# Kernel optimization log

Hardware: AMD Instinct MI355X
Metric: run time of the kernel (lower is better)

The kernel has to match this reference:

```python
import jax, jax.numpy as jnp
import numpy as np

N = 80000       # nodes
E = 1280000     # edges (avg degree 16)
G = 2000        # graphs
NSHAPE, NCOLOR, POSMAX = 16, 16, 1024
HID, OUT, IN_DIM = 64, 2, 40
EPS = 1e-5


def setup_inputs() -> dict:
    key = jax.random.key(0)
    ks = jax.random.split(key, 20)
    f32 = jnp.float32
    return {
        "shape_id": jax.random.randint(ks[0], (N,), 0, NSHAPE),
        "color_id": jax.random.randint(ks[1], (N,), 0, NCOLOR),
        "pos_id": jax.random.randint(ks[2], (N,), 0, POSMAX),
        "edge_index": jax.random.randint(ks[3], (2, E), 0, N),
        "batch": jnp.sort(jax.random.randint(ks[4], (N,), 0, G)),
        "num_graphs": G,
        "shape_tab": jax.random.normal(ks[5], (NSHAPE, 16), f32),
        "color_tab": jax.random.normal(ks[6], (NCOLOR, 16), f32),
        "pos_tab": jax.random.normal(ks[7], (POSMAX, 8), f32),
        "W1l": jax.random.normal(ks[8], (IN_DIM, HID), f32) / np.sqrt(IN_DIM),
        "b1": jnp.zeros((HID,), f32),
        "W1r": jax.random.normal(ks[9], (IN_DIM, HID), f32) / np.sqrt(IN_DIM),
        "g1": jnp.ones((HID,), f32),
        "be1": jnp.zeros((HID,), f32),
        "W2l": jax.random.normal(ks[10], (HID, HID), f32) / np.sqrt(HID),
        "b2": jnp.zeros((HID,), f32),
        "W2r": jax.random.normal(ks[11], (HID, HID), f32) / np.sqrt(HID),
        "g2": jnp.ones((HID,), f32),
        "be2": jnp.zeros((HID,), f32),
        "Wout": jax.random.normal(ks[12], (HID, OUT), f32) / np.sqrt(HID),
        "bout": jnp.zeros((OUT,), f32),
    }


def sage_conv(x, src, dst, Wl, b, Wr, n_nodes):
    # PyG SAGEConv (mean aggr): out = lin_l(mean_{j in N(i)} x_j) + lin_r(x_i)
    agg = jax.ops.segment_sum(x[src], dst, num_segments=n_nodes)     # [N, F]
    deg = jax.ops.segment_sum(jnp.ones((src.shape[0], 1), x.dtype), dst,
                              num_segments=n_nodes)                  # [N, 1]
    agg = agg / jnp.maximum(deg, 1.0)
    return agg @ Wl + b + x @ Wr


def batch_norm(x, gamma, beta):
    # training-mode BatchNorm1d over nodes
    m = x.mean(axis=0)
    v = x.var(axis=0)
    return (x - m) * (gamma / jnp.sqrt(v + EPS)) + beta


def reference(shape_id, color_id, pos_id, edge_index, batch, num_graphs,
              shape_tab, color_tab, pos_tab,
              W1l, b1, W1r, g1, be1,
              W2l, b2, W2r, g2, be2,
              Wout, bout):
    n_nodes = shape_id.shape[0]
    src, dst = edge_index[0], edge_index[1]
    x = jnp.concatenate([shape_tab[shape_id], color_tab[color_id],
                         pos_tab[pos_id]], axis=-1)                  # [N, 40]
    x = jax.nn.relu(batch_norm(sage_conv(x, src, dst, W1l, b1, W1r, n_nodes), g1, be1))
    # dropout: eval mode -> identity
    x = jax.nn.relu(batch_norm(sage_conv(x, src, dst, W2l, b2, W2r, n_nodes), g2, be2))
    # global mean pool over batch segments
    summed = jax.ops.segment_sum(x, batch, num_segments=num_graphs)   # [G, H]
    counts = jax.ops.segment_sum(jnp.ones((n_nodes, 1), x.dtype), batch,
                                 num_segments=num_graphs)
    pooled = summed / jnp.maximum(counts, 1.0)
    return pooled @ Wout + bout                                       # [G, 2]
```

## Files before the change

kernel.cpp:

```cpp
#include <hip/hip_runtime.h>

#define NN 80000
#define NE 1280000
#define NG 2000
#define HID 64
#define FIN1 40
#define NBUK ((NN + 127) >> 7)
#define BIN_PER 4096
constexpr float EPS = 1e-5f;

typedef _Float16 f16;
typedef f16 f16x4 __attribute__((ext_vector_type(4)));
typedef f16 f16x8 __attribute__((ext_vector_type(8)));
typedef float f32x4 __attribute__((ext_vector_type(4)));

__global__ void embed16(const int* __restrict__ sid, const int* __restrict__ cid,
                        const int* __restrict__ pid,
                        const float* __restrict__ stab, const float* __restrict__ ctab,
                        const float* __restrict__ ptab, f16* __restrict__ x0) {
    int idx = blockIdx.x * 256 + threadIdx.x;
    if (idx >= NN * 5) return;
    int n = idx / 5, u = idx - n * 5;
    const float* srcp;
    if (u < 2)      srcp = &stab[sid[n] * 16 + u * 8];
    else if (u < 4) srcp = &ctab[cid[n] * 16 + (u - 2) * 8];
    else            srcp = &ptab[pid[n] * 8];
    f16x8 o;
#pragma unroll
    for (int i = 0; i < 8; i++) o[i] = (f16)srcp[i];
    *(f16x8*)&x0[(size_t)n * FIN1 + u * 8] = o;
}

__global__ void wprep(const float* __restrict__ W1l, const float* __restrict__ W1r,
                      const float* __restrict__ W2l, const float* __restrict__ W2r,
                      f16* __restrict__ Bt1, f16* __restrict__ Bt2) {
    int i = blockIdx.x * 256 + threadIdx.x;
    if (i < 64 * 104) {
        int j = i / 104, k = i - j * 104;
        float v = 0.f;
        if (k < 40) v = W1l[k * 64 + j];
        else if (k < 80) v = W1r[(k - 40) * 64 + j];
        Bt1[i] = (f16)v;
    }
    int i2 = i - 64 * 104;
    if (i2 >= 0 && i2 < 64 * 136) {
        int j = i2 / 136, k = i2 - j * 136;
        float v = 0.f;
        if (k < 64) v = W2l[k * 64 + j];
        else if (k < 128) v = W2r[(k - 64) * 64 + j];
        Bt2[i2] = (f16)v;
    }
}

__global__ void bucket_hist(const int* __restrict__ dst, int* __restrict__ bcnt) {
    __shared__ int lh[NBUK];
    for (int i = threadIdx.x; i < NBUK; i += 256) lh[i] = 0;
    __syncthreads();
    int e0 = blockIdx.x * BIN_PER;
    int e1 = min(e0 + BIN_PER, NE);
    for (int e = e0 + threadIdx.x; e < e1; e += 256) atomicAdd(&lh[dst[e] >> 7], 1);
    __syncthreads();
    for (int i = threadIdx.x; i < NBUK; i += 256)
        if (lh[i]) atomicAdd(&bcnt[i], lh[i]);
}

__global__ void bucket_scan(const int* __restrict__ bcnt, int* __restrict__ bstart,
                            int* __restrict__ bcur) {
    __shared__ int l[1024];
    int t = threadIdx.x;
    l[t] = (t < NBUK) ? bcnt[t] : 0;
    __syncthreads();
    for (int off = 1; off < 1024; off <<= 1) {
        int v = (t >= off) ? l[t - off] : 0;
        __syncthreads();
        l[t] += v;
        __syncthreads();
    }
    int excl = (t == 0) ? 0 : l[t - 1];
    if (t < NBUK) { bstart[t] = excl; bcur[t] = excl; }
    if (t == NBUK) bstart[NBUK] = NE;
}

__global__ void bin_edges(const int* __restrict__ src, const int* __restrict__ dst,
                          int* __restrict__ bcur, int* __restrict__ ebuf) {
    __shared__ int lh[NBUK];
    __shared__ int lbase[NBUK];
    for (int i = threadIdx.x; i < NBUK; i += 256) lh[i] = 0;
    __syncthreads();
    int e0 = blockIdx.x * BIN_PER;
    int e1 = min(e0 + BIN_PER, NE);
    for (int e = e0 + threadIdx.x; e < e1; e += 256) atomicAdd(&lh[dst[e] >> 7], 1);
    __syncthreads();
    for (int i = threadIdx.x; i < NBUK; i += 256) {
        int c = lh[i];
        lbase[i] = c ? atomicAdd(&bcur[i], c) : 0;
    }
    __syncthreads();
    for (int i = threadIdx.x; i < NBUK; i += 256) lh[i] = 0;
    __syncthreads();
    for (int e = e0 + threadIdx.x; e < e1; e += 256) {
        int d = dst[e];
        int b = d >> 7;
        int off = atomicAdd(&lh[b], 1);
        ebuf[lbase[b] + off] = (src[e] << 7) | (d & 127);
    }
}

__global__ void csr_fill2(const int* __restrict__ ebuf, const int* __restrict__ bstart,
                          int* __restrict__ row_ptr, int* __restrict__ eidx) {
    __shared__ int cnt[128];
    __shared__ int sb[128];
    __shared__ int lcur[128];
    int b = blockIdx.x;
    int t = threadIdx.x;
    int nbase = b << 7;
    if (t < 128) cnt[t] = 0;
    __syncthreads();
    int s0 = bstart[b], s1 = bstart[b + 1];
    for (int i = s0 + t; i < s1; i += 256) atomicAdd(&cnt[ebuf[i] & 127], 1);
    __syncthreads();
    if (t < 128) sb[t] = cnt[t];
    __syncthreads();
    for (int off = 1; off < 128; off <<= 1) {
        int v = (t >= off && t < 128) ? sb[t - off] : 0;
        __syncthreads();
        if (t < 128) sb[t] += v;
        __syncthreads();
    }
    if (t < 128) {
        int excl = ((t == 0) ? 0 : sb[t - 1]) + s0;
        row_ptr[nbase + t] = excl;
        lcur[t] = excl;
    }
    if (b == 0 && t == 0) row_ptr[NN] = NE;
    __syncthreads();
    for (int i = s0 + t; i < s1; i += 256) {
        int v = ebuf[i];
        int pos = atomicAdd(&lcur[v & 127], 1);
        eidx[pos] = v >> 7;
    }
}

template <int F>
__global__ void gather16(const int* __restrict__ row_ptr, const int* __restrict__ eidx,
                         const f16* __restrict__ x, f16* __restrict__ agg) {
    int t = blockIdx.x * blockDim.x + threadIdx.x;
    int n = t >> 6;
    int lane = threadIdx.x & 63;
    if (n >= NN) return;
    int grp = lane >> 3;
    int fl = (lane & 7) * 8;
    bool active = fl < F;
    int beg = row_ptr[n], end = row_ptr[n + 1];
    float ac[8];
#pragma unroll
    for (int i = 0; i < 8; i++) ac[i] = 0.f;
    for (int j0 = beg; j0 < end; j0 += 64) {
        int cnt = min(64, end - j0);
        int myid = (j0 + lane < end) ? eidx[j0 + lane] : 0;
        int steps = (cnt + 7) >> 3;
        for (int u = 0; u < steps; u++) {
            int e = u * 8 + grp;
            int s = __shfl(myid, e);
            if (e < cnt && active) {
                f16x8 v = *(const f16x8*)&x[(size_t)s * F + fl];
#pragma unroll
                for (int i = 0; i < 8; i++) ac[i] += (float)v[i];
            }
        }
    }
#pragma unroll
    for (int m = 8; m <= 32; m <<= 1) {
#pragma unroll
        for (int i = 0; i < 8; i++) ac[i] += __shfl_xor(ac[i], m);
    }
    if (lane < 8 && active) {
        f16x8 o;
#pragma unroll
        for (int i = 0; i < 8; i++) o[i] = (f16)ac[i];
        *(f16x8*)&agg[(size_t)n * F + fl] = o;
    }
}

template <int FIN, int KTOT, int KP>
__launch_bounds__(256)
__global__ void sage_mfma(const f16* __restrict__ x, const f16* __restrict__ agg,
                          const int* __restrict__ row_ptr, const f16* __restrict__ Btg,
                          const float* __restrict__ bias, f16* __restrict__ h) {
    __shared__ f16 Asm[64 * KP];
    __shared__ f16 Bsm[64 * KP];
    __shared__ float sinv[64];

    int tid = threadIdx.x;
    int n0 = blockIdx.x * 64;

    if (tid < 64) {
        int n = n0 + tid;
        int deg = row_ptr[n + 1] - row_ptr[n];
        sinv[tid] = 1.0f / (float)max(deg, 1);
    }
    __syncthreads();

    constexpr int UA = FIN / 8;
    constexpr int UT = KP / 8;
    for (int i = tid; i < 64 * UT; i += 256) {
        int r = i / UT, u = i - r * UT;
        f16x8 o;
        if (u < UA) {
            f16x8 va = *(const f16x8*)&agg[(size_t)(n0 + r) * FIN + u * 8];
            float inv = sinv[r];
#pragma unroll
            for (int k = 0; k < 8; k++) o[k] = (f16)((float)va[k] * inv);
        } else if (u < 2 * UA) {
            o = *(const f16x8*)&x[(size_t)(n0 + r) * FIN + (u - UA) * 8];
        } else {
#pragma unroll
            for (int k = 0; k < 8; k++) o[k] = (f16)0.f;
        }
        *(f16x8*)&Asm[r * KP + u * 8] = o;
    }
    const int NU4 = 64 * KP * 2 / 16;
    for (int i = tid; i < NU4; i += 256)
        ((uint4*)Bsm)[i] = ((const uint4*)Btg)[i];
    __syncthreads();

    int w = tid >> 6;
    int l = tid & 63;
    int jloc = l & 15;
    int kg = l >> 4;
    int rbase = w * 16;

    f32x4 acc[4];
#pragma unroll
    for (int jt = 0; jt < 4; jt++) {
        float bj = bias[jt * 16 + jloc];
        acc[jt] = (f32x4){bj, bj, bj, bj};
    }
#pragma unroll
    for (int kk = 0; kk < KTOT / 32; kk++) {
        f16x8 af = *(const f16x8*)&Asm[(rbase + jloc) * KP + kk * 32 + kg * 8];
#pragma unroll
        for (int jt = 0; jt < 4; jt++) {
            f16x8 bf = *(const f16x8*)&Bsm[(jt * 16 + jloc) * KP + kk * 32 + kg * 8];
            acc[jt] = __builtin_amdgcn_mfma_f32_16x16x32_f16(af, bf, acc[jt], 0, 0, 0);
        }
    }
#pragma unroll
    for (int jt = 0; jt < 4; jt++) {
#pragma unroll
        for (int reg = 0; reg < 4; reg++) {
            int n = n0 + rbase + kg * 4 + reg;
            h[(size_t)n * HID + jt * 16 + jloc] = (f16)acc[jt][reg];
        }
    }
}

__global__ void bn_stats16(const f16* __restrict__ h, float* __restrict__ stats) {
    const int NPB = 512;
    int f = threadIdx.x & 63;
    int r = threadIdx.x >> 6;
    int n0 = blockIdx.x * NPB;
    int nend = min(n0 + NPB, NN);
    float s = 0.f, ss = 0.f;
    for (int n = n0 + r; n < nend; n += 4) {
        float v = (float)h[(size_t)n * HID + f];
        s += v;
        ss += v * v;
    }
    __shared__ float ls[4][64];
    __shared__ float lss[4][64];
    ls[r][f] = s;
    lss[r][f] = ss;
    __syncthreads();
    if (r == 0) {
        s = ls[0][f] + ls[1][f] + ls[2][f] + ls[3][f];
        ss = lss[0][f] + lss[1][f] + lss[2][f] + lss[3][f];
        atomicAdd(&stats[f], s);
        atomicAdd(&stats[64 + f], ss);
    }
}

__global__ void bn_apply16(f16* __restrict__ h, const float* __restrict__ stats,
                           const float* __restrict__ g, const float* __restrict__ be) {
    __shared__ float ssc[64], ssh[64];
    int tid = threadIdx.x;
    if (tid < 64) {
        const float invn = 1.0f / (float)NN;
        float m = stats[tid] * invn;
        float var = stats[64 + tid] * invn - m * m;
        float sc = g[tid] * __frsqrt_rn(var + EPS);
        ssc[tid] = sc;
        ssh[tid] = be[tid] - m * sc;
    }
    __syncthreads();
    int idx = blockIdx.x * 256 + tid;
    if (idx >= NN * 8) return;
    int f = (idx & 7) * 8;
    f16x8 v = *(f16x8*)&h[(size_t)idx * 8];
    f16x8 o;
#pragma unroll
    for (int i = 0; i < 8; i++) {
        float xv = (float)v[i];
        o[i] = (f16)fmaxf(fmaf(xv, ssc[f + i], ssh[f + i]), 0.f);
    }
    *(f16x8*)&h[(size_t)idx * 8] = o;
}

__global__ void graph_bounds(const int* __restrict__ batch, int* __restrict__ gstart) {
    int n = blockIdx.x * blockDim.x + threadIdx.x;
    if (n >= NN) return;
    int cur = batch[n];
    int prev = (n == 0) ? -1 : batch[n - 1];
    for (int g = prev + 1; g <= cur; g++) gstart[g] = n;
    if (n == NN - 1) {
        for (int g = cur + 1; g <= NG; g++) gstart[g] = NN;
    }
}

__global__ void pool_out(const f16* __restrict__ h, const float* __restrict__ stats2,
                         const float* __restrict__ g2, const float* __restrict__ be2,
                         const int* __restrict__ gstart,
                         const float* __restrict__ Wout, const float* __restrict__ bout,
                         float* __restrict__ out) {
    int w = (blockIdx.x * blockDim.x + threadIdx.x) >> 6;
    int f = threadIdx.x & 63;
    if (w >= NG) return;
    const float invn = 1.0f / (float)NN;
    float m = stats2[f] * invn;
    float var = stats2[64 + f] * invn - m * m;
    float sc = g2[f] / sqrtf(var + EPS);
    float sh = be2[f] - m * sc;
    int n0 = gstart[w], n1 = gstart[w + 1];
    float acc = 0.f;
    for (int n = n0; n < n1; n++) {
        float v = fmaf((float)h[(size_t)n * HID + f], sc, sh);
        acc += fmaxf(v, 0.0f);
    }
    float inv = 1.0f / (float)max(n1 - n0, 1);
    float p = acc * inv;
    float a0 = p * Wout[f * 2 + 0];
    float a1 = p * Wout[f * 2 + 1];
#pragma unroll
    for (int mm = 1; mm < 64; mm <<= 1) {
        a0 += __shfl_xor(a0, mm);
        a1 += __shfl_xor(a1, mm);
    }
    if (f == 0) {
        out[w * 2 + 0] = a0 + bout[0];
        out[w * 2 + 1] = a1 + bout[1];
    }
}

extern "C" void kernel_launch(void* const* d_in, const int* in_sizes, int n_in,
                              void* d_out, int out_size, void* d_ws, size_t ws_size,
                              hipStream_t stream) {
    const int* sid = (const int*)d_in[0];
    const int* cid = (const int*)d_in[1];
    const int* pid = (const int*)d_in[2];
    const int* ei = (const int*)d_in[3];
    const int* batch = (const int*)d_in[4];
    const float* stab = (const float*)d_in[6];
    const float* ctab = (const float*)d_in[7];
    const float* ptab = (const float*)d_in[8];
    const float* W1l = (const float*)d_in[9];
    const float* b1 = (const float*)d_in[10];
    const float* W1r = (const float*)d_in[11];
    const float* g1 = (const float*)d_in[12];
    const float* be1 = (const float*)d_in[13];
    const float* W2l = (const float*)d_in[14];
    const float* b2 = (const float*)d_in[15];
    const float* W2r = (const float*)d_in[16];
    const float* g2 = (const float*)d_in[17];
    const float* be2 = (const float*)d_in[18];
    const float* Wout = (const float*)d_in[19];
    const float* bout = (const float*)d_in[20];

    const int* src = ei;
    const int* dst = ei + NE;

    char* p = (char*)d_ws;
    f16* x0 = (f16*)p;        p += (size_t)NN * FIN1 * 2;
    f16* agg = (f16*)p;       p += (size_t)NN * HID * 2;
    f16* h1 = (f16*)p;        p += (size_t)NN * HID * 2;
    f16* h2 = (f16*)p;        p += (size_t)NN * HID * 2;
    float* stats = (float*)p; p += 256 * 4;
    f16* bt1 = (f16*)p;       p += 64 * 104 * 2;
    f16* bt2 = (f16*)p;       p += 64 * 136 * 2;
    int* row_ptr = (int*)p;   p += (NN + 1) * 4;
    int* gstart = (int*)p;    p += (NG + 1) * 4;
    int* bcnt = (int*)p;      p += NBUK * 4;
    int* bstart = (int*)p;    p += (NBUK + 1) * 4;
    int* bcur = (int*)p;      p += NBUK * 4;
    int* eidx = (int*)p;      p += (size_t)NE * 4;
    int* ebuf = (int*)p;      p += (size_t)NE * 4;

    hipMemsetAsync(bcnt, 0, NBUK * sizeof(int), stream);
    hipMemsetAsync(stats, 0, 256 * sizeof(float), stream);

    const int B = 256;

    embed16<<<(NN * 5 + B - 1) / B, B, 0, stream>>>(sid, cid, pid, stab, ctab, ptab, x0);
    wprep<<<60, B, 0, stream>>>(W1l, W1r, W2l, W2r, bt1, bt2);

    bucket_hist<<<(NE + BIN_PER - 1) / BIN_PER, B, 0, stream>>>(dst, bcnt);
    bucket_scan<<<1, 1024, 0, stream>>>(bcnt, bstart, bcur);
    bin_edges<<<(NE + BIN_PER - 1) / BIN_PER, B, 0, stream>>>(src, dst, bcur, ebuf);
    csr_fill2<<<NBUK, B, 0, stream>>>(ebuf, bstart, row_ptr, eidx);

    graph_bounds<<<(NN + B - 1) / B, B, 0, stream>>>(batch, gstart);

    gather16<FIN1><<<(NN * 64 + B - 1) / B, B, 0, stream>>>(row_ptr, eidx, x0, agg);
    sage_mfma<FIN1, 96, 104><<<NN / 64, B, 0, stream>>>(x0, agg, row_ptr, bt1, b1, h1);
    bn_stats16<<<(NN + 511) / 512, B, 0, stream>>>(h1, stats);
    bn_apply16<<<(NN * 8 + B - 1) / B, B, 0, stream>>>(h1, stats, g1, be1);

    gather16<HID><<<(NN * 64 + B - 1) / B, B, 0, stream>>>(row_ptr, eidx, h1, agg);
    sage_mfma<HID, 128, 136><<<NN / 64, B, 0, stream>>>(h1, agg, row_ptr, bt2, b2, h2);
    bn_stats16<<<(NN + 511) / 512, B, 0, stream>>>(h2, stats + 128);

    pool_out<<<(NG * 64 + B - 1) / B, B, 0, stream>>>(h2, stats + 128, g2, be2, gstart,
                                                      Wout, bout, (float*)d_out);
}
```

Before: 261.4 us.

## Fuse setup kernels, pack embedding ids, and rebuild CSR with deterministic per-block offsets

Merges embedding id packing, weight prep, graph bounds and f16 table conversion into one setup kernel. The materialized x0 feature matrix is dropped: the first gather and the first MFMA layer read packed ids and look up small f16 tables directly. The CSR build moves to 256-node buckets, with per-block histograms and a scan that precomputes each block's offsets, so global atomics and one histogram pass go away. In exchange there are extra indirect lookups per edge and a serial per-bucket loop over blocks in a single-block scan.

```diff
diff --git a/kernel.cpp b/kernel.cpp
--- a/kernel.cpp
+++ b/kernel.cpp
@@ -5,147 +5,198 @@
 #define NG 2000
 #define HID 64
 #define FIN1 40
-#define NBUK ((NN + 127) >> 7)
-#define BIN_PER 4096
+#define BSZ 256
+#define NBUK ((NN + BSZ - 1) / BSZ)
+#define NBS 320
+#define EB 8192
+#define NBB ((NE + EB - 1) / EB)
 constexpr float EPS = 1e-5f;
 
 typedef _Float16 f16;
-typedef f16 f16x4 __attribute__((ext_vector_type(4)));
 typedef f16 f16x8 __attribute__((ext_vector_type(8)));
 typedef float f32x4 __attribute__((ext_vector_type(4)));
 
-__global__ void embed16(const int* __restrict__ sid, const int* __restrict__ cid,
-                        const int* __restrict__ pid,
-                        const float* __restrict__ stab, const float* __restrict__ ctab,
-                        const float* __restrict__ ptab, f16* __restrict__ x0) {
-    int idx = blockIdx.x * 256 + threadIdx.x;
-    if (idx >= NN * 5) return;
-    int n = idx / 5, u = idx - n * 5;
-    const float* srcp;
-    if (u < 2)      srcp = &stab[sid[n] * 16 + u * 8];
-    else if (u < 4) srcp = &ctab[cid[n] * 16 + (u - 2) * 8];
-    else            srcp = &ptab[pid[n] * 8];
-    f16x8 o;
-#pragma unroll
-    for (int i = 0; i < 8; i++) o[i] = (f16)srcp[i];
-    *(f16x8*)&x0[(size_t)n * FIN1 + u * 8] = o;
-}
-
-__global__ void wprep(const float* __restrict__ W1l, const float* __restrict__ W1r,
+__global__ void setup(const int* __restrict__ sid, const int* __restrict__ cid,
+                      const int* __restrict__ pid, const int* __restrict__ batch,
+                      const float* __restrict__ stab, const float* __restrict__ ctab,
+                      const float* __restrict__ ptab,
+                      const float* __restrict__ W1l, const float* __restrict__ W1r,
                       const float* __restrict__ W2l, const float* __restrict__ W2r,
-                      f16* __restrict__ Bt1, f16* __restrict__ Bt2) {
-    int i = blockIdx.x * 256 + threadIdx.x;
-    if (i < 64 * 104) {
-        int j = i / 104, k = i - j * 104;
-        float v = 0.f;
-        if (k < 40) v = W1l[k * 64 + j];
-        else if (k < 80) v = W1r[(k - 40) * 64 + j];
-        Bt1[i] = (f16)v;
-    }
-    int i2 = i - 64 * 104;
-    if (i2 >= 0 && i2 < 64 * 136) {
-        int j = i2 / 136, k = i2 - j * 136;
-        float v = 0.f;
-        if (k < 64) v = W2l[k * 64 + j];
-        else if (k < 128) v = W2r[(k - 64) * 64 + j];
-        Bt2[i2] = (f16)v;
-    }
-}
-
-__global__ void bucket_hist(const int* __restrict__ dst, int* __restrict__ bcnt) {
+                      int* __restrict__ ids, f16* __restrict__ Bt1, f16* __restrict__ Bt2,
+                      int* __restrict__ gstart,
+                      f16* __restrict__ stab16, f16* __restrict__ ctab16,
+                      f16* __restrict__ ptab16) {
+    int bid = blockIdx.x;
+    int tid = threadIdx.x;
+    if (bid < 313) {
+        int n = bid * 256 + tid;
+        if (n < NN) ids[n] = sid[n] | (cid[n] << 4) | (pid[n] << 8);
+    } else if (bid < 373) {
+        int i = (bid - 313) * 256 + tid;
+        if (i < 64 * 104) {
+            int j = i / 104, k = i - j * 104;
+            float v = 0.f;
+            if (k < 40) v = W1l[k * 64 + j];
+            else if (k < 80) v = W1r[(k - 40) * 64 + j];
+            Bt1[i] = (f16)v;
+        }
+        int i2 = i - 64 * 104;
+        if (i2 >= 0 && i2 < 64 * 136) {
+            int j = i2 / 136, k = i2 - j * 136;
+            float v = 0.f;
+            if (k < 64) v = W2l[k * 64 + j];
+            else if (k < 128) v = W2r[(k - 64) * 64 + j];
+            Bt2[i2] = (f16)v;
+        }
+    } else if (bid < 686) {
+        int n = (bid - 373) * 256 + tid;
+        if (n >= NN) return;
+        int cur = batch[n];
+        int prev = (n == 0) ? -1 : batch[n - 1];
+        for (int g = prev + 1; g <= cur; g++) gstart[g] = n;
+        if (n == NN - 1)
+            for (int g = cur + 1; g <= NG; g++) gstart[g] = NN;
+    } else {
+        int i = (bid - 686) * 256 + tid;
+        if (i < 256) stab16[i] = (f16)stab[i];
+        else if (i < 512) ctab16[i - 256] = (f16)ctab[i - 256];
+        else if (i < 512 + 8192) ptab16[i - 512] = (f16)ptab[i - 512];
+    }
+}
+
+__global__ void khist(const int* __restrict__ dst, int* __restrict__ bhist) {
     __shared__ int lh[NBUK];
     for (int i = threadIdx.x; i < NBUK; i += 256) lh[i] = 0;
     __syncthreads();
-    int e0 = blockIdx.x * BIN_PER;
-    int e1 = min(e0 + BIN_PER, NE);
-    for (int e = e0 + threadIdx.x; e < e1; e += 256) atomicAdd(&lh[dst[e] >> 7], 1);
-    __syncthreads();
-    for (int i = threadIdx.x; i < NBUK; i += 256)
-        if (lh[i]) atomicAdd(&bcnt[i], lh[i]);
-}
-
-__global__ void bucket_scan(const int* __restrict__ bcnt, int* __restrict__ bstart,
-                            int* __restrict__ bcur) {
-    __shared__ int l[1024];
+    int e0 = blockIdx.x * EB, e1 = min(e0 + EB, NE);
+    for (int e = e0 + threadIdx.x; e < e1; e += 256) atomicAdd(&lh[dst[e] >> 8], 1);
+    __syncthreads();
+    for (int i = threadIdx.x; i < NBUK; i += 256) bhist[blockIdx.x * NBS + i] = lh[i];
+}
+
+__global__ void kscan(const int* __restrict__ bhist, int* __restrict__ bstart,
+                      int* __restrict__ lbase_all) {
+    __shared__ int l[512];
     int t = threadIdx.x;
-    l[t] = (t < NBUK) ? bcnt[t] : 0;
-    __syncthreads();
-    for (int off = 1; off < 1024; off <<= 1) {
+    int total = 0;
+    if (t < NBUK)
+        for (int blk = 0; blk < NBB; blk++) total += bhist[blk * NBS + t];
+    l[t] = (t < NBUK) ? total : 0;
+    __syncthreads();
+    for (int off = 1; off < 512; off <<= 1) {
         int v = (t >= off) ? l[t - off] : 0;
         __syncthreads();
         l[t] += v;
         __syncthreads();
     }
     int excl = (t == 0) ? 0 : l[t - 1];
-    if (t < NBUK) { bstart[t] = excl; bcur[t] = excl; }
+    if (t < NBUK) {
+        bstart[t] = excl;
+        int run = excl;
+        for (int blk = 0; blk < NBB; blk++) {
+            lbase_all[blk * NBS + t] = run;
+            run += bhist[blk * NBS + t];
+        }
+    }
     if (t == NBUK) bstart[NBUK] = NE;
 }
 
-__global__ void bin_edges(const int* __restrict__ src, const int* __restrict__ dst,
-                          int* __restrict__ bcur, int* __restrict__ ebuf) {
-    __shared__ int lh[NBUK];
-    __shared__ int lbase[NBUK];
-    for (int i = threadIdx.x; i < NBUK; i += 256) lh[i] = 0;
-    __syncthreads();
-    int e0 = blockIdx.x * BIN_PER;
-    int e1 = min(e0 + BIN_PER, NE);
-    for (int e = e0 + threadIdx.x; e < e1; e += 256) atomicAdd(&lh[dst[e] >> 7], 1);
-    __syncthreads();
-    for (int i = threadIdx.x; i < NBUK; i += 256) {
-        int c = lh[i];
-        lbase[i] = c ? atomicAdd(&bcur[i], c) : 0;
-    }
-    __syncthreads();
-    for (int i = threadIdx.x; i < NBUK; i += 256) lh[i] = 0;
-    __syncthreads();
+__global__ void kbin(const int* __restrict__ src, const int* __restrict__ dst,
+                     const int* __restrict__ lbase_all, int* __restrict__ ebuf) {
+    __shared__ int lcur[NBUK];
+    for (int i = threadIdx.x; i < NBUK; i += 256) lcur[i] = lbase_all[blockIdx.x * NBS + i];
+    __syncthreads();
+    int e0 = blockIdx.x * EB, e1 = min(e0 + EB, NE);
     for (int e = e0 + threadIdx.x; e < e1; e += 256) {
         int d = dst[e];
-        int b = d >> 7;
-        int off = atomicAdd(&lh[b], 1);
-        ebuf[lbase[b] + off] = (src[e] << 7) | (d & 127);
-    }
-}
-
-__global__ void csr_fill2(const int* __restrict__ ebuf, const int* __restrict__ bstart,
-                          int* __restrict__ row_ptr, int* __restrict__ eidx) {
-    __shared__ int cnt[128];
-    __shared__ int sb[128];
-    __shared__ int lcur[128];
-    int b = blockIdx.x;
-    int t = threadIdx.x;
-    int nbase = b << 7;
-    if (t < 128) cnt[t] = 0;
+        int off = atomicAdd(&lcur[d >> 8], 1);
+        ebuf[off] = (src[e] << 8) | (d & 255);
+    }
+}
+
+__global__ void kfill(const int* __restrict__ ebuf, const int* __restrict__ bstart,
+                      int* __restrict__ row_ptr, int* __restrict__ eidx) {
+    __shared__ int cnt[BSZ];
+    __shared__ int sb[BSZ];
+    __shared__ int lcur[BSZ];
+    int b = blockIdx.x, t = threadIdx.x;
+    int nbase = b << 8;
+    cnt[t] = 0;
     __syncthreads();
     int s0 = bstart[b], s1 = bstart[b + 1];
-    for (int i = s0 + t; i < s1; i += 256) atomicAdd(&cnt[ebuf[i] & 127], 1);
-    __syncthreads();
-    if (t < 128) sb[t] = cnt[t];
-    __syncthreads();
-    for (int off = 1; off < 128; off <<= 1) {
-        int v = (t >= off && t < 128) ? sb[t - off] : 0;
+    for (int i = s0 + t; i < s1; i += 256) atomicAdd(&cnt[ebuf[i] & 255], 1);
+    __syncthreads();
+    sb[t] = cnt[t];
+    __syncthreads();
+    for (int off = 1; off < BSZ; off <<= 1) {
+        int v = (t >= off) ? sb[t - off] : 0;
         __syncthreads();
-        if (t < 128) sb[t] += v;
+        sb[t] += v;
         __syncthreads();
     }
-    if (t < 128) {
-        int excl = ((t == 0) ? 0 : sb[t - 1]) + s0;
-        row_ptr[nbase + t] = excl;
-        lcur[t] = excl;
-    }
+    int excl = ((t == 0) ? 0 : sb[t - 1]) + s0;
+    int n = nbase + t;
+    if (n < NN) row_ptr[n] = excl;
+    lcur[t] = excl;
     if (b == 0 && t == 0) row_ptr[NN] = NE;
     __syncthreads();
     for (int i = s0 + t; i < s1; i += 256) {
         int v = ebuf[i];
-        int pos = atomicAdd(&lcur[v & 127], 1);
-        eidx[pos] = v >> 7;
+        int pos = atomicAdd(&lcur[v & 255], 1);
+        eidx[pos] = v >> 8;
+    }
+}
+
+__global__ void gather1(const int* __restrict__ row_ptr, const int* __restrict__ eidx,
+                        const int* __restrict__ ids,
+                        const f16* __restrict__ stab16, const f16* __restrict__ ctab16,
+                        const f16* __restrict__ ptab16, f16* __restrict__ agg) {
+    int tt = blockIdx.x * 256 + threadIdx.x;
+    int n = tt >> 6;
+    int lane = threadIdx.x & 63;
+    if (n >= NN) return;
+    int grp = lane >> 3, li = lane & 7;
+    int beg = row_ptr[n], end = row_ptr[n + 1];
+    float ac[8];
+#pragma unroll
+    for (int i = 0; i < 8; i++) ac[i] = 0.f;
+    for (int j0 = beg; j0 < end; j0 += 64) {
+        int cnt = min(64, end - j0);
+        int myid = (j0 + lane < end) ? eidx[j0 + lane] : 0;
+        int steps = (cnt + 7) >> 3;
+        for (int u = 0; u < steps; u++) {
+            int e = u * 8 + grp;
+            int s = __shfl(myid, e);
+            if (e < cnt && li < 5) {
+                int id = ids[s];
+                const f16* rowp;
+                if (li < 2)      rowp = &stab16[(id & 15) * 16 + li * 8];
+                else if (li < 4) rowp = &ctab16[((id >> 4) & 15) * 16 + (li - 2) * 8];
+                else             rowp = &ptab16[(id >> 8) * 8];
+                f16x8 v = *(const f16x8*)rowp;
+#pragma unroll
+                for (int i = 0; i < 8; i++) ac[i] += (float)v[i];
+            }
+        }
+    }
+#pragma unroll
+    for (int m = 8; m <= 32; m <<= 1) {
+#pragma unroll
+        for (int i = 0; i < 8; i++) ac[i] += __shfl_xor(ac[i], m);
+    }
+    if (lane < 5) {
+        f16x8 o;
+#pragma unroll
+        for (int i = 0; i < 8; i++) o[i] = (f16)ac[i];
+        *(f16x8*)&agg[(size_t)n * FIN1 + lane * 8] = o;
     }
 }
 
 template <int F>
 __global__ void gather16(const int* __restrict__ row_ptr, const int* __restrict__ eidx,
                          const f16* __restrict__ x, f16* __restrict__ agg) {
-    int t = blockIdx.x * blockDim.x + threadIdx.x;
-    int n = t >> 6;
+    int tt = blockIdx.x * 256 + threadIdx.x;
+    int n = tt >> 6;
     int lane = threadIdx.x & 63;
     if (n >= NN) return;
     int grp = lane >> 3;
@@ -182,18 +233,20 @@
     }
 }
 
-template <int FIN, int KTOT, int KP>
 __launch_bounds__(256)
-__global__ void sage_mfma(const f16* __restrict__ x, const f16* __restrict__ agg,
-                          const int* __restrict__ row_ptr, const f16* __restrict__ Btg,
-                          const float* __restrict__ bias, f16* __restrict__ h) {
+__global__ void sage_mfma1(const int* __restrict__ ids, const f16* __restrict__ agg,
+                           const int* __restrict__ row_ptr,
+                           const f16* __restrict__ stab16, const f16* __restrict__ ctab16,
+                           const f16* __restrict__ ptab16,
+                           const f16* __restrict__ Btg, const float* __restrict__ bias,
+                           f16* __restrict__ h) {
+    const int KTOT = 96, KP = 104, UT = KP / 8;
     __shared__ f16 Asm[64 * KP];
     __shared__ f16 Bsm[64 * KP];
     __shared__ float sinv[64];
 
     int tid = threadIdx.x;
     int n0 = blockIdx.x * 64;
-
     if (tid < 64) {
         int n = n0 + tid;
         int deg = row_ptr[n + 1] - row_ptr[n];
@@ -201,35 +254,35 @@
     }
     __syncthreads();
 
-    constexpr int UA = FIN / 8;
-    constexpr int UT = KP / 8;
     for (int i = tid; i < 64 * UT; i += 256) {
         int r = i / UT, u = i - r * UT;
         f16x8 o;
-        if (u < UA) {
-            f16x8 va = *(const f16x8*)&agg[(size_t)(n0 + r) * FIN + u * 8];
+        if (u < 5) {
+            f16x8 va = *(const f16x8*)&agg[(size_t)(n0 + r) * FIN1 + u * 8];
             float inv = sinv[r];
 #pragma unroll
             for (int k = 0; k < 8; k++) o[k] = (f16)((float)va[k] * inv);
-        } else if (u < 2 * UA) {
-            o = *(const f16x8*)&x[(size_t)(n0 + r) * FIN + (u - UA) * 8];
+        } else if (u < 10) {
+            int id = ids[n0 + r];
+            int c = u - 5;
+            const f16* rowp;
+            if (c < 2)      rowp = &stab16[(id & 15) * 16 + c * 8];
+            else if (c < 4) rowp = &ctab16[((id >> 4) & 15) * 16 + (c - 2) * 8];
+            else            rowp = &ptab16[(id >> 8) * 8];
+            o = *(const f16x8*)rowp;
         } else {
 #pragma unroll
             for (int k = 0; k < 8; k++) o[k] = (f16)0.f;
         }
         *(f16x8*)&Asm[r * KP + u * 8] = o;
     }
-    const int NU4 = 64 * KP * 2 / 16;
-    for (int i = tid; i < NU4; i += 256)
+    for (int i = tid; i < 64 * KP * 2 / 16; i += 256)
         ((uint4*)Bsm)[i] = ((const uint4*)Btg)[i];
     __syncthreads();
 
-    int w = tid >> 6;
-    int l = tid & 63;
-    int jloc = l & 15;
-    int kg = l >> 4;
+    int w = tid >> 6, l = tid & 63;
+    int jloc = l & 15, kg = l >> 4;
     int rbase = w * 16;
-
     f32x4 acc[4];
 #pragma unroll
     for (int jt = 0; jt < 4; jt++) {
@@ -246,13 +299,77 @@
         }
     }
 #pragma unroll
-    for (int jt = 0; jt < 4; jt++) {
+    for (int jt = 0; jt < 4; jt++)
 #pragma unroll
         for (int reg = 0; reg < 4; reg++) {
             int n = n0 + rbase + kg * 4 + reg;
             h[(size_t)n * HID + jt * 16 + jloc] = (f16)acc[jt][reg];
         }
-    }
+}
+
+__launch_bounds__(256)
+__global__ void sage_mfma2(const f16* __restrict__ x, const f16* __restrict__ agg,
+                           const int* __restrict__ row_ptr, const f16* __restrict__ Btg,
+                           const float* __restrict__ bias, f16* __restrict__ h) {
+    const int FIN = 64, KTOT = 128, KP = 136, UT = KP / 8;
+    __shared__ f16 Asm[64 * KP];
+    __shared__ f16 Bsm[64 * KP];
+    __shared__ float sinv[64];
+
+    int tid = threadIdx.x;
+    int n0 = blockIdx.x * 64;
+    if (tid < 64) {
+        int n = n0 + tid;
+        int deg = row_ptr[n + 1] - row_ptr[n];
+        sinv[tid] = 1.0f / (float)max(deg, 1);
+    }
+    __syncthreads();
+
+    for (int i = tid; i < 64 * UT; i += 256) {
+        int r = i / UT, u = i - r * UT;
+        f16x8 o;
+        if (u < 8) {
+            f16x8 va = *(const f16x8*)&agg[(size_t)(n0 + r) * FIN + u * 8];
+            float inv = sinv[r];
+#pragma unroll
+            for (int k = 0; k < 8; k++) o[k] = (f16)((float)va[k] * inv);
+        } else if (u < 16) {
+            o = *(const f16x8*)&x[(size_t)(n0 + r) * FIN + (u - 8) * 8];
+        } else {
+#pragma unroll
+            for (int k = 0; k < 8; k++) o[k] = (f16)0.f;
+        }
+        *(f16x8*)&Asm[r * KP + u * 8] = o;
+    }
+    for (int i = tid; i < 64 * KP * 2 / 16; i += 256)
+        ((uint4*)Bsm)[i] = ((const uint4*)Btg)[i];
+    __syncthreads();
+
+    int w = tid >> 6, l = tid & 63;
+    int jloc = l & 15, kg = l >> 4;
+    int rbase = w * 16;
+    f32x4 acc[4];
+#pragma unroll
+    for (int jt = 0; jt < 4; jt++) {
+        float bj = bias[jt * 16 + jloc];
+        acc[jt] = (f32x4){bj, bj, bj, bj};
+    }
+#pragma unroll
+    for (int kk = 0; kk < KTOT / 32; kk++) {
+        f16x8 af = *(const f16x8*)&Asm[(rbase + jloc) * KP + kk * 32 + kg * 8];
+#pragma unroll
+        for (int jt = 0; jt < 4; jt++) {
+            f16x8 bf = *(const f16x8*)&Bsm[(jt * 16 + jloc) * KP + kk * 32 + kg * 8];
+            acc[jt] = __builtin_amdgcn_mfma_f32_16x16x32_f16(af, bf, acc[jt], 0, 0, 0);
+        }
+    }
+#pragma unroll
+    for (int jt = 0; jt < 4; jt++)
+#pragma unroll
+        for (int reg = 0; reg < 4; reg++) {
+            int n = n0 + rbase + kg * 4 + reg;
+            h[(size_t)n * HID + jt * 16 + jloc] = (f16)acc[jt][reg];
+        }
 }
 
 __global__ void bn_stats16(const f16* __restrict__ h, float* __restrict__ stats) {
@@ -304,17 +421,6 @@
         o[i] = (f16)fmaxf(fmaf(xv, ssc[f + i], ssh[f + i]), 0.f);
     }
     *(f16x8*)&h[(size_t)idx * 8] = o;
-}
-
-__global__ void graph_bounds(const int* __restrict__ batch, int* __restrict__ gstart) {
-    int n = blockIdx.x * blockDim.x + threadIdx.x;
-    if (n >= NN) return;
-    int cur = batch[n];
-    int prev = (n == 0) ? -1 : batch[n - 1];
-    for (int g = prev + 1; g <= cur; g++) gstart[g] = n;
-    if (n == NN - 1) {
-        for (int g = cur + 1; g <= NG; g++) gstart[g] = NN;
-    }
 }
 
 __global__ void pool_out(const f16* __restrict__ h, const float* __restrict__ stats2,
@@ -379,43 +485,46 @@
     const int* dst = ei + NE;
 
     char* p = (char*)d_ws;
-    f16* x0 = (f16*)p;        p += (size_t)NN * FIN1 * 2;
-    f16* agg = (f16*)p;       p += (size_t)NN * HID * 2;
-    f16* h1 = (f16*)p;        p += (size_t)NN * HID * 2;
-    f16* h2 = (f16*)p;        p += (size_t)NN * HID * 2;
-    float* stats = (float*)p; p += 256 * 4;
-    f16* bt1 = (f16*)p;       p += 64 * 104 * 2;
-    f16* bt2 = (f16*)p;       p += 64 * 136 * 2;
-    int* row_ptr = (int*)p;   p += (NN + 1) * 4;
-    int* gstart = (int*)p;    p += (NG + 1) * 4;
-    int* bcnt = (int*)p;      p += NBUK * 4;
-    int* bstart = (int*)p;    p += (NBUK + 1) * 4;
-    int* bcur = (int*)p;      p += NBUK * 4;
-    int* eidx = (int*)p;      p += (size_t)NE * 4;
-    int* ebuf = (int*)p;      p += (size_t)NE * 4;
-
-    hipMemsetAsync(bcnt, 0, NBUK * sizeof(int), stream);
+    f16* agg = (f16*)p;        p += (size_t)NN * HID * 2;
+    f16* h1 = (f16*)p;         p += (size_t)NN * HID * 2;
+    f16* h2 = (f16*)p;         p += (size_t)NN * HID * 2;
+    f16* bt1 = (f16*)p;        p += 64 * 104 * 2;
+    f16* bt2 = (f16*)p;        p += 64 * 136 * 2;
+    f16* stab16 = (f16*)p;     p += 256 * 2;
+    f16* ctab16 = (f16*)p;     p += 256 * 2;
+    f16* ptab16 = (f16*)p;     p += 8192 * 2;
+    float* stats = (float*)p;  p += 256 * 4;
+    int* ids = (int*)p;        p += (size_t)NN * 4;
+    int* row_ptr = (int*)p;    p += (NN + 1) * 4;
+    int* gstart = (int*)p;     p += (NG + 1) * 4;
+    int* bhist = (int*)p;      p += (size_t)NBB * NBS * 4;
+    int* lbase = (int*)p;      p += (size_t)NBB * NBS * 4;
+    int* bstart = (int*)p;     p += (NBUK + 1) * 4;
+    int* eidx = (int*)p;       p += (size_t)NE * 4;
+    int* ebuf = (int*)p;       p += (size_t)NE * 4;
+
     hipMemsetAsync(stats, 0, 256 * sizeof(float), stream);
 
     const int B = 256;
 
-    embed16<<<(NN * 5 + B - 1) / B, B, 0, stream>>>(sid, cid, pid, stab, ctab, ptab, x0);
-    wprep<<<60, B, 0, stream>>>(W1l, W1r, W2l, W2r, bt1, bt2);
-
-    bucket_hist<<<(NE + BIN_PER - 1) / BIN_PER, B, 0, stream>>>(dst, bcnt);
-    bucket_scan<<<1, 1024, 0, stream>>>(bcnt, bstart, bcur);
-    bin_edges<<<(NE + BIN_PER - 1) / BIN_PER, B, 0, stream>>>(src, dst, bcur, ebuf);
-    csr_fill2<<<NBUK, B, 0, stream>>>(ebuf, bstart, row_ptr, eidx);
-
-    graph_bounds<<<(NN + B - 1) / B, B, 0, stream>>>(batch, gstart);
-
-    gather16<FIN1><<<(NN * 64 + B - 1) / B, B, 0, stream>>>(row_ptr, eidx, x0, agg);
-    sage_mfma<FIN1, 96, 104><<<NN / 64, B, 0, stream>>>(x0, agg, row_ptr, bt1, b1, h1);
+    setup<<<720, B, 0, stream>>>(sid, cid, pid, batch, stab, ctab, ptab,
+                                 W1l, W1r, W2l, W2r,
+                                 ids, bt1, bt2, gstart, stab16, ctab16, ptab16);
+
+    khist<<<NBB, B, 0, stream>>>(dst, bhist);
+    kscan<<<1, 512, 0, stream>>>(bhist, bstart, lbase);
+    kbin<<<NBB, B, 0, stream>>>(src, dst, lbase, ebuf);
+    kfill<<<NBUK, B, 0, stream>>>(ebuf, bstart, row_ptr, eidx);
+
+    gather1<<<(NN * 64 + B - 1) / B, B, 0, stream>>>(row_ptr, eidx, ids,
+                                                     stab16, ctab16, ptab16, agg);
+    sage_mfma1<<<NN / 64, B, 0, stream>>>(ids, agg, row_ptr, stab16, ctab16, ptab16,
+                                          bt1, b1, h1);
     bn_stats16<<<(NN + 511) / 512, B, 0, stream>>>(h1, stats);
     bn_apply16<<<(NN * 8 + B - 1) / B, B, 0, stream>>>(h1, stats, g1, be1);
 
     gather16<HID><<<(NN * 64 + B - 1) / B, B, 0, stream>>>(row_ptr, eidx, h1, agg);
-    sage_mfma<HID, 128, 136><<<NN / 64, B, 0, stream>>>(h1, agg, row_ptr, bt2, b2, h2);
+    sage_mfma2<<<NN / 64, B, 0, stream>>>(h1, agg, row_ptr, bt2, b2, h2);
     bn_stats16<<<(NN + 511) / 512, B, 0, stream>>>(h2, stats + 128);
 
     pool_out<<<(NG * 64 + B - 1) / B, B, 0, stream>>>(h2, stats + 128, g2, be2, gstart,
```

After: 249.4 us. -4.6%, faster.
